# Performance work log

Hardware: AMD Instinct MI355X
Metric: run time of the kernel (lower is better)

The kernel has to match this reference:

```python
import jax, jax.numpy as jnp
import numpy as np

N, D = 8192, 1024


def setup_inputs() -> dict:
    key = jax.random.key(0)
    k1, k2, k3, k4 = jax.random.split(key, 4)
    return {
        "first_features": jax.random.normal(k1, (N, D), dtype=jnp.float32),
        "second_features": jax.random.normal(k2, (N, D), dtype=jnp.float32),
        "first_label": jax.random.randint(k3, (N,), 0, N, dtype=jnp.int64),
        "second_label": jax.random.randint(k4, (N,), 0, N, dtype=jnp.int64),
        "logit_scale": jnp.asarray(10.0, dtype=jnp.float32),
        "logit_bias": jnp.asarray(-10.0, dtype=jnp.float32),
    }


def reference(first_features, second_features, first_label, second_label,
              logit_scale, logit_bias):
    # logits: [N, N] = scale * A @ B^T + bias
    logits = logit_scale * jnp.einsum("id,jd->ij", first_features, second_features)
    logits = logits + logit_bias
    # ground truth: +1 where labels match, -1 elsewhere
    labels = jnp.where(first_label[:, None] == second_label[None, :], 1.0, -1.0)
    labels = labels.astype(logits.dtype)
    # loss = sum(-logsigmoid(labels * logits)) / N  (mask_diagonal=False)
    loss = -jnp.sum(jax.nn.log_sigmoid(labels * logits)) / first_features.shape[0]
    return loss
```

## Files before the change

kernel.cpp:

```cpp
#include <hip/hip_runtime.h>
#include <hip/hip_bf16.h>
#include <stdint.h>

#define N_TOK 8192
#define D_K   1024
#define NB    128
#define BKF   128
#define NT    (D_K / BKF)
#define TILE_B (NB * BKF)

typedef __attribute__((ext_vector_type(4))) int   i32x4;
typedef __attribute__((ext_vector_type(8))) int   i32x8;
typedef __attribute__((ext_vector_type(4))) float f32x4;

__global__ void zero_out_kernel(float* out) { out[0] = 0.0f; }

__device__ __forceinline__ unsigned int f32_to_e4m3(float x) {
  uint32_t u = __builtin_bit_cast(uint32_t, x);
  unsigned int s = (u >> 24) & 0x80u;
  float ax = __builtin_fabsf(x);
  if (ax < 0.015625f) {
    int q = (int)rintf(ax * 512.0f);
    return s | (unsigned int)q;
  }
  uint32_t au = u & 0x7FFFFFFFu;
  uint32_t v = au + 0x7FFFFu + ((au >> 20) & 1u);
  int em = (int)(v >> 20) - 960;
  if (em > 0x7E) em = 0x7E;
  return s | (unsigned int)em;
}

__global__ void __launch_bounds__(256)
convert_kernel(const float* __restrict__ a, const float* __restrict__ b,
               unsigned int* __restrict__ oa, unsigned int* __restrict__ ob) {
  const size_t total4 = (size_t)N_TOK * D_K / 4;
  size_t i = (size_t)blockIdx.x * blockDim.x + threadIdx.x;
  size_t stride = (size_t)gridDim.x * blockDim.x;
  for (; i < total4; i += stride) {
    float4 va = ((const float4*)a)[i];
    float4 vb = ((const float4*)b)[i];
    oa[i] = f32_to_e4m3(va.x) | (f32_to_e4m3(va.y) << 8) |
            (f32_to_e4m3(va.z) << 16) | (f32_to_e4m3(va.w) << 24);
    ob[i] = f32_to_e4m3(vb.x) | (f32_to_e4m3(vb.y) << 8) |
            (f32_to_e4m3(vb.z) << 16) | (f32_to_e4m3(vb.w) << 24);
  }
}

__global__ void __launch_bounds__(256)
sigc_kernel(const unsigned char* __restrict__ A8,
            const unsigned char* __restrict__ B8,
            const int* __restrict__ labA, const int* __restrict__ labB,
            const float* __restrict__ scale_p, const float* __restrict__ bias_p,
            float* __restrict__ out) {
  __shared__ unsigned char sA[2][TILE_B];
  __shared__ unsigned char sB[2][TILE_B];
  __shared__ int sLabA[NB];
  __shared__ int sLabB[NB];
  __shared__ float sPart[4];

  const int tid  = threadIdx.x;
  const int lane = tid & 63;
  const int wid  = tid >> 6;
  const int wr   = wid >> 1;
  const int wc   = wid & 1;
  const int lr   = lane & 15;
  const int kq   = lane >> 4;

  const int bid = (int)blockIdx.x;
  const int xcd = bid & 7;
  const int ii  = bid >> 3;
  const int rr  = (xcd >> 1) * 16 + (ii & 15);
  const int cc  = (xcd & 1) * 32 + (ii >> 4);
  const int bRow = rr * NB;
  const int bCol = cc * NB;

  if (tid < 128)      sLabA[tid] = labA[bRow + tid];
  else                sLabB[tid - 128] = labB[bCol + (tid - 128)];

  auto stageOp = [&](const unsigned char* __restrict__ G, int gBase,
                     unsigned char* dst, int t) {
#pragma unroll
    for (int ld = 0; ld < 4; ++ld) {
      const int e    = ld * 4096 + tid * 16;
      const int row  = e >> 7;
      const int slot = (e >> 4) & 7;
      const int col  = (slot ^ (row & 7)) << 4;
      const unsigned char* g =
          G + (size_t)(gBase + row) * D_K + t * BKF + col;
      __builtin_amdgcn_global_load_lds(
          (const __attribute__((address_space(1))) void*)g,
          (__attribute__((address_space(3))) void*)(dst + ld * 4096 + wid * 1024),
          16, 0, 0);
    }
  };

  f32x4 acc[4][4];
#pragma unroll
  for (int i = 0; i < 4; ++i)
#pragma unroll
    for (int j = 0; j < 4; ++j) acc[i][j] = (f32x4){0.f, 0.f, 0.f, 0.f};

  stageOp(A8, bRow, sA[0], 0); stageOp(B8, bCol, sB[0], 0);
  stageOp(A8, bRow, sA[1], 1); stageOp(B8, bCol, sB[1], 1);
  asm volatile("s_waitcnt vmcnt(16)" ::: "memory");
  __syncthreads();

  for (int t = 0; t < NT; ++t) {
    const unsigned char* pA = sA[t & 1];
    const unsigned char* pB = sB[t & 1];

    i32x8 afr[4], bfr[4];
#pragma unroll
    for (int f = 0; f < 4; ++f) {
      {
        const int r = wr * 64 + f * 16 + lr;
        const int s0 = 2 * kq, s1 = 2 * kq + 1;
        i32x4 lo = *(const i32x4*)&pA[r * BKF + ((s0 ^ (r & 7)) << 4)];
        i32x4 hi = *(const i32x4*)&pA[r * BKF + ((s1 ^ (r & 7)) << 4)];
        afr[f] = __builtin_shufflevector(lo, hi, 0, 1, 2, 3, 4, 5, 6, 7);
      }
      {
        const int r = wc * 64 + f * 16 + lr;
        const int s0 = 2 * kq, s1 = 2 * kq + 1;
        i32x4 lo = *(const i32x4*)&pB[r * BKF + ((s0 ^ (r & 7)) << 4)];
        i32x4 hi = *(const i32x4*)&pB[r * BKF + ((s1 ^ (r & 7)) << 4)];
        bfr[f] = __builtin_shufflevector(lo, hi, 0, 1, 2, 3, 4, 5, 6, 7);
      }
    }

#pragma unroll
    for (int mf = 0; mf < 4; ++mf)
#pragma unroll
      for (int nf = 0; nf < 4; ++nf)
        acc[mf][nf] = __builtin_amdgcn_mfma_scale_f32_16x16x128_f8f6f4(
            afr[mf], bfr[nf], acc[mf][nf], 0, 0,
            0, 0x7F7F7F7F, 0, 0x7F7F7F7F);

    if (t < NT - 1) {
      __builtin_amdgcn_sched_barrier(0);
      __builtin_amdgcn_s_barrier();
      if (t < NT - 2) {
        stageOp(A8, bRow, sA[t & 1], t + 2);
        stageOp(B8, bCol, sB[t & 1], t + 2);
        asm volatile("s_waitcnt vmcnt(16)" ::: "memory");
      } else {
        asm volatile("s_waitcnt vmcnt(0)" ::: "memory");
      }
      __builtin_amdgcn_sched_barrier(0);
      __builtin_amdgcn_s_barrier();
    }
  }

  const float L2E = 1.4426950408889634f;
  const float sl2e = scale_p[0] * L2E;
  const float bl2e = bias_p[0] * L2E;
  float loss = 0.0f;
  const int cBase = lane & 15;
  const int rBase = (lane >> 4) * 4;
#pragma unroll
  for (int mf = 0; mf < 4; ++mf)
#pragma unroll
    for (int nf = 0; nf < 4; ++nf) {
      const int colL = sLabB[wc * 64 + nf * 16 + cBase];
#pragma unroll
      for (int r = 0; r < 4; ++r) {
        const int rowL = sLabA[wr * 64 + mf * 16 + rBase + r];
        const float u0 = fmaf(sl2e, acc[mf][nf][r], bl2e);
        const float u = (rowL == colL) ? -u0 : u0;
        loss += fmaxf(u, 0.0f) + log2f(1.0f + exp2f(-fabsf(u)));
      }
    }

#pragma unroll
  for (int off = 32; off > 0; off >>= 1) loss += __shfl_down(loss, off, 64);
  if (lane == 0) sPart[wid] = loss;
  __syncthreads();
  if (tid == 0) {
    const float s = (sPart[0] + sPart[1]) + (sPart[2] + sPart[3]);
    atomicAdd(out, s * (0.6931471805599453f / (float)N_TOK));
  }
}

extern "C" void kernel_launch(void* const* d_in, const int* in_sizes, int n_in,
                              void* d_out, int out_size, void* d_ws, size_t ws_size,
                              hipStream_t stream) {
  const float* a  = (const float*)d_in[0];
  const float* b  = (const float*)d_in[1];
  const int*   la = (const int*)d_in[2];
  const int*   lb = (const int*)d_in[3];
  const float* sc = (const float*)d_in[4];
  const float* bi = (const float*)d_in[5];
  float* out = (float*)d_out;

  unsigned char* wa = (unsigned char*)d_ws;
  unsigned char* wb = wa + (size_t)N_TOK * D_K;

  zero_out_kernel<<<1, 1, 0, stream>>>(out);
  convert_kernel<<<2048, 256, 0, stream>>>(a, b, (unsigned int*)wa,
                                           (unsigned int*)wb);
  const int grid = (N_TOK / NB) * (N_TOK / NB);
  sigc_kernel<<<grid, 256, 0, stream>>>(wa, wb, la, lb, sc, bi, out);
}
```

Measured before the change: 120.8 us.

## Load FP8 MFMA fragments directly from global into registers, dropping LDS staging

The main loop no longer stages A/B tiles through shared memory with global_load_lds and barriers. Each wave now loads its MFMA operand fragments straight from global memory into registers, double-buffered, and wraps the MFMAs in s_setprio. Launch bounds request two blocks per CU. This removes LDS traffic and block-wide barriers, but redundant operand fetches (A rows are shared by two waves, B rows likewise) now go to L1/L2. Doubled fragment registers may also pressure occupancy.

```diff
diff --git a/kernel.cpp b/kernel.cpp
--- a/kernel.cpp
+++ b/kernel.cpp
@@ -7,9 +7,7 @@
 #define NB    128
 #define BKF   128
 #define NT    (D_K / BKF)
-#define TILE_B (NB * BKF)
 
-typedef __attribute__((ext_vector_type(4))) int   i32x4;
 typedef __attribute__((ext_vector_type(8))) int   i32x8;
 typedef __attribute__((ext_vector_type(4))) float f32x4;
 
@@ -46,14 +44,12 @@
   }
 }
 
-__global__ void __launch_bounds__(256)
+__global__ void __launch_bounds__(256, 2)
 sigc_kernel(const unsigned char* __restrict__ A8,
             const unsigned char* __restrict__ B8,
             const int* __restrict__ labA, const int* __restrict__ labB,
             const float* __restrict__ scale_p, const float* __restrict__ bias_p,
             float* __restrict__ out) {
-  __shared__ unsigned char sA[2][TILE_B];
-  __shared__ unsigned char sB[2][TILE_B];
   __shared__ int sLabA[NB];
   __shared__ int sLabB[NB];
   __shared__ float sPart[4];
@@ -76,23 +72,12 @@
 
   if (tid < 128)      sLabA[tid] = labA[bRow + tid];
   else                sLabB[tid - 128] = labB[bCol + (tid - 128)];
+  __syncthreads();
 
-  auto stageOp = [&](const unsigned char* __restrict__ G, int gBase,
-                     unsigned char* dst, int t) {
-#pragma unroll
-    for (int ld = 0; ld < 4; ++ld) {
-      const int e    = ld * 4096 + tid * 16;
-      const int row  = e >> 7;
-      const int slot = (e >> 4) & 7;
-      const int col  = (slot ^ (row & 7)) << 4;
-      const unsigned char* g =
-          G + (size_t)(gBase + row) * D_K + t * BKF + col;
-      __builtin_amdgcn_global_load_lds(
-          (const __attribute__((address_space(1))) void*)g,
-          (__attribute__((address_space(3))) void*)(dst + ld * 4096 + wid * 1024),
-          16, 0, 0);
-    }
-  };
+  const unsigned char* aBase =
+      A8 + (size_t)(bRow + wr * 64 + lr) * D_K + kq * 32;
+  const unsigned char* bBase =
+      B8 + (size_t)(bCol + wc * 64 + lr) * D_K + kq * 32;
 
   f32x4 acc[4][4];
 #pragma unroll
@@ -100,55 +85,32 @@
 #pragma unroll
     for (int j = 0; j < 4; ++j) acc[i][j] = (f32x4){0.f, 0.f, 0.f, 0.f};
 
-  stageOp(A8, bRow, sA[0], 0); stageOp(B8, bCol, sB[0], 0);
-  stageOp(A8, bRow, sA[1], 1); stageOp(B8, bCol, sB[1], 1);
-  asm volatile("s_waitcnt vmcnt(16)" ::: "memory");
-  __syncthreads();
+  i32x8 fA0[4], fB0[4], fA1[4], fB1[4];
 
-  for (int t = 0; t < NT; ++t) {
-    const unsigned char* pA = sA[t & 1];
-    const unsigned char* pB = sB[t & 1];
+#define LOADT(fa, fb, t) do {                                              \
+    _Pragma("unroll") for (int _f = 0; _f < 4; ++_f) {                     \
+      fa[_f] = *(const i32x8*)(aBase + (size_t)_f * 16 * D_K + (t) * BKF); \
+      fb[_f] = *(const i32x8*)(bBase + (size_t)_f * 16 * D_K + (t) * BKF); \
+    } } while (0)
 
-    i32x8 afr[4], bfr[4];
-#pragma unroll
-    for (int f = 0; f < 4; ++f) {
-      {
-        const int r = wr * 64 + f * 16 + lr;
-        const int s0 = 2 * kq, s1 = 2 * kq + 1;
-        i32x4 lo = *(const i32x4*)&pA[r * BKF + ((s0 ^ (r & 7)) << 4)];
-        i32x4 hi = *(const i32x4*)&pA[r * BKF + ((s1 ^ (r & 7)) << 4)];
-        afr[f] = __builtin_shufflevector(lo, hi, 0, 1, 2, 3, 4, 5, 6, 7);
-      }
-      {
-        const int r = wc * 64 + f * 16 + lr;
-        const int s0 = 2 * kq, s1 = 2 * kq + 1;
-        i32x4 lo = *(const i32x4*)&pB[r * BKF + ((s0 ^ (r & 7)) << 4)];
-        i32x4 hi = *(const i32x4*)&pB[r * BKF + ((s1 ^ (r & 7)) << 4)];
-        bfr[f] = __builtin_shufflevector(lo, hi, 0, 1, 2, 3, 4, 5, 6, 7);
-      }
-    }
+#define MMAT(fa, fb) do {                                                  \
+    __builtin_amdgcn_s_setprio(1);                                         \
+    _Pragma("unroll") for (int _mf = 0; _mf < 4; ++_mf)                    \
+    _Pragma("unroll") for (int _nf = 0; _nf < 4; ++_nf)                    \
+      acc[_mf][_nf] = __builtin_amdgcn_mfma_scale_f32_16x16x128_f8f6f4(    \
+          fa[_mf], fb[_nf], acc[_mf][_nf], 0, 0,                           \
+          0, 0x7F7F7F7F, 0, 0x7F7F7F7F);                                   \
+    __builtin_amdgcn_s_setprio(0); } while (0)
+
+  LOADT(fA0, fB0, 0);
 
 #pragma unroll
-    for (int mf = 0; mf < 4; ++mf)
-#pragma unroll
-      for (int nf = 0; nf < 4; ++nf)
-        acc[mf][nf] = __builtin_amdgcn_mfma_scale_f32_16x16x128_f8f6f4(
-            afr[mf], bfr[nf], acc[mf][nf], 0, 0,
-            0, 0x7F7F7F7F, 0, 0x7F7F7F7F);
-
-    if (t < NT - 1) {
-      __builtin_amdgcn_sched_barrier(0);
-      __builtin_amdgcn_s_barrier();
-      if (t < NT - 2) {
-        stageOp(A8, bRow, sA[t & 1], t + 2);
-        stageOp(B8, bCol, sB[t & 1], t + 2);
-        asm volatile("s_waitcnt vmcnt(16)" ::: "memory");
-      } else {
-        asm volatile("s_waitcnt vmcnt(0)" ::: "memory");
-      }
-      __builtin_amdgcn_sched_barrier(0);
-      __builtin_amdgcn_s_barrier();
-    }
+  for (int t2 = 0; t2 < NT / 2; ++t2) {
+    const int e = 2 * t2;
+    LOADT(fA1, fB1, e + 1);
+    MMAT(fA0, fB0);
+    if (t2 < NT / 2 - 1) LOADT(fA0, fB0, e + 2);
+    MMAT(fA1, fB1);
   }
 
   const float L2E = 1.4426950408889634f;
```

Result: slower. 253.2 us (+109.6%).
